# Kernel optimization log

Hardware: AMD Instinct MI355X
Metric: run time of the kernel (lower is better)

## Reference

```python
import jax, jax.numpy as jnp
import numpy as np


def setup_inputs() -> dict:
    key = jax.random.key(0)
    k1, k2, k3 = jax.random.split(key, 3)
    B, H, I, O, Dp1 = 4, 2048, 1024, 1024, 4  # degree=3 -> degree+1=4
    x = jax.random.normal(k1, (B, H, I, Dp1), dtype=jnp.float32)
    weight = 0.1 * jax.random.normal(k2, (O, Dp1), dtype=jnp.float32)
    weighted_sum = 0.1 * jax.random.normal(k3, (O, I), dtype=jnp.float32)
    return {"x": x, "weight": weight, "weighted_sum": weighted_sum}


def reference(x, weight, weighted_sum):
    # Original: weights[o,i,d] = weighted_sum[o,i] * weight[o,d];
    #           out[b,h,o] = sum_{i,d} x[b,h,i,d] * weights[o,i,d]
    # Fused 3-operand einsum avoids materializing the (O, I, D+1) intermediate.
    return jnp.einsum('bhid,oi,od->bho', x, weighted_sum, weight)
```

## Files before the change

### kernel.cpp

```cpp
#include <hip/hip_runtime.h>

typedef unsigned short u16;
typedef u16 u16x4 __attribute__((ext_vector_type(4)));
typedef float f32x4 __attribute__((ext_vector_type(4)));
typedef __bf16 bf16x8 __attribute__((ext_vector_type(8)));

#define M_DIM 8192
#define N_DIM 1024
#define K_DIM 4096

__device__ __forceinline__ u16 f2bf(float f) {
  unsigned u = __float_as_uint(f);
  u += 0x7FFFu + ((u >> 16) & 1u);
  return (u16)(u >> 16);
}

__global__ __launch_bounds__(256) void k_cvt(const float* __restrict__ x,
                                             u16* __restrict__ y) {
  long i = ((long)blockIdx.x * 256 + threadIdx.x) * 4;
  f32x4 a = *(const f32x4*)(x + i);
  u16x4 r;
  r[0] = f2bf(a[0]); r[1] = f2bf(a[1]); r[2] = f2bf(a[2]); r[3] = f2bf(a[3]);
  *(u16x4*)(y + i) = r;
}

__global__ __launch_bounds__(256) void k_w2(const float* __restrict__ w,
                                            const float* __restrict__ ws,
                                            u16* __restrict__ w2) {
  int idx = blockIdx.x * 256 + threadIdx.x;
  int o = idx >> 10;
  float s = ws[idx];
  f32x4 wv = *(const f32x4*)(w + o * 4);
  u16x4 r;
  r[0] = f2bf(s * wv[0]); r[1] = f2bf(s * wv[1]);
  r[2] = f2bf(s * wv[2]); r[3] = f2bf(s * wv[3]);
  *(u16x4*)(w2 + (size_t)idx * 4) = r;
}

typedef __attribute__((address_space(1))) const void gvoid_t;
typedef __attribute__((address_space(3))) void lvoid_t;
__device__ __forceinline__ void gll16(const void* g, void* l) {
  __builtin_amdgcn_global_load_lds((gvoid_t*)g, (lvoid_t*)l, 16, 0, 0);
}

__global__ __launch_bounds__(512) void k_gemm(const u16* __restrict__ A,
                                              const u16* __restrict__ Bt,
                                              float* __restrict__ C) {
  __shared__ u16 sA[128 * 64];
  __shared__ u16 sB[128 * 64];

  const int t    = threadIdx.x;
  const int lane = t & 63;
  const int wid  = t >> 6;
  const int m0   = blockIdx.y * 128;
  const int n0   = blockIdx.x * 128;

  const int s0 = t, s1 = t + 512;
  const int r0 = s0 >> 3, c0 = (s0 & 7) ^ (r0 & 7);
  const int r1 = s1 >> 3, c1 = (s1 & 7) ^ (r1 & 7);
  const u16* gA0 = A  + (size_t)(m0 + r0) * K_DIM + c0 * 8;
  const u16* gA1 = A  + (size_t)(m0 + r1) * K_DIM + c1 * 8;
  const u16* gB0 = Bt + (size_t)(n0 + r0) * K_DIM + c0 * 8;
  const u16* gB1 = Bt + (size_t)(n0 + r1) * K_DIM + c1 * 8;
  u16* lA0 = sA + s0 * 8;  u16* lA1 = sA + s1 * 8;
  u16* lB0 = sB + s0 * 8;  u16* lB1 = sB + s1 * 8;

  const int wm = (wid >> 1) * 32;
  const int wn = (wid & 1) * 64;
  const int fr = lane & 15;
  const int lc = lane >> 4;

  f32x4 acc[2][4];
#pragma unroll
  for (int i = 0; i < 2; i++)
#pragma unroll
    for (int j = 0; j < 4; j++) acc[i][j] = (f32x4){0.f, 0.f, 0.f, 0.f};

  for (int k0 = 0; k0 < K_DIM; k0 += 64) {
    gll16(gA0, lA0); gll16(gA1, lA1);
    gll16(gB0, lB0); gll16(gB1, lB1);
    gA0 += 64; gA1 += 64; gB0 += 64; gB1 += 64;
    __syncthreads();

#pragma unroll
    for (int ks = 0; ks < 2; ks++) {
      bf16x8 af[2], bf[4];
#pragma unroll
      for (int mi = 0; mi < 2; mi++) {
        int r  = wm + mi * 16 + fr;
        int pc = (ks * 4 + lc) ^ (r & 7);
        af[mi] = *(const bf16x8*)(sA + r * 64 + pc * 8);
      }
#pragma unroll
      for (int ni = 0; ni < 4; ni++) {
        int r  = wn + ni * 16 + fr;
        int pc = (ks * 4 + lc) ^ (r & 7);
        bf[ni] = *(const bf16x8*)(sB + r * 64 + pc * 8);
      }
#pragma unroll
      for (int mi = 0; mi < 2; mi++)
#pragma unroll
        for (int ni = 0; ni < 4; ni++)
          acc[mi][ni] = __builtin_amdgcn_mfma_f32_16x16x32_bf16(
              af[mi], bf[ni], acc[mi][ni], 0, 0, 0);
    }
    __syncthreads();
  }

  const int cr = (lane >> 4) * 4;
  const int cc = lane & 15;
#pragma unroll
  for (int mi = 0; mi < 2; mi++)
#pragma unroll
    for (int ni = 0; ni < 4; ni++) {
      float* cp = C + (size_t)(m0 + wm + mi * 16 + cr) * N_DIM +
                  (n0 + wn + ni * 16 + cc);
#pragma unroll
      for (int r = 0; r < 4; r++) cp[(size_t)r * N_DIM] = acc[mi][ni][r];
    }
}

extern "C" void kernel_launch(void* const* d_in, const int* in_sizes, int n_in,
                              void* d_out, int out_size, void* d_ws, size_t ws_size,
                              hipStream_t stream) {
  const float* x  = (const float*)d_in[0];
  const float* w  = (const float*)d_in[1];
  const float* ws = (const float*)d_in[2];
  float* out = (float*)d_out;

  u16* xbf = (u16*)d_ws;
  u16* w2  = xbf + (size_t)M_DIM * K_DIM;

  k_cvt<<<32768, 256, 0, stream>>>(x, xbf);
  k_w2<<<4096, 256, 0, stream>>>(w, ws, w2);

  dim3 grid(N_DIM / 128, M_DIM / 128);
  k_gemm<<<grid, 512, 0, stream>>>(xbf, w2, out);
}
```

Baseline: 279.5 us.

## Split K across wave pairs in GEMM with LDS reduction of partial sums

The GEMM block now gives each wave a 64x64 output tile instead of 32x64, with the two halves of each 64-wide K slice handled by separate wave groups. The partial accumulators are then summed through shared memory before the store. This halves the LDS fragment loads per MFMA and raises register-level reuse. In exchange it adds a reduction step, more accumulator registers, a larger shared buffer (64KB) and a launch-bounds occupancy hint.

After: 279.8 us. About the same (+0.1%).

```diff
diff --git a/kernel.cpp b/kernel.cpp
--- a/kernel.cpp
+++ b/kernel.cpp
@@ -43,11 +43,12 @@
   __builtin_amdgcn_global_load_lds((gvoid_t*)g, (lvoid_t*)l, 16, 0, 0);
 }
 
-__global__ __launch_bounds__(512) void k_gemm(const u16* __restrict__ A,
-                                              const u16* __restrict__ Bt,
-                                              float* __restrict__ C) {
-  __shared__ u16 sA[128 * 64];
-  __shared__ u16 sB[128 * 64];
+__global__ __launch_bounds__(512, 4) void k_gemm(const u16* __restrict__ A,
+                                                 const u16* __restrict__ Bt,
+                                                 float* __restrict__ C) {
+  __shared__ u16 smem[32768];
+  u16* sA = smem;
+  u16* sB = smem + 8192;
 
   const int t    = threadIdx.x;
   const int lane = t & 63;
@@ -65,14 +66,15 @@
   u16* lA0 = sA + s0 * 8;  u16* lA1 = sA + s1 * 8;
   u16* lB0 = sB + s0 * 8;  u16* lB1 = sB + s1 * 8;
 
-  const int wm = (wid >> 1) * 32;
-  const int wn = (wid & 1) * 64;
+  const int kh = wid >> 2;
+  const int wm = (wid & 1) * 64;
+  const int wn = ((wid >> 1) & 1) * 64;
   const int fr = lane & 15;
   const int lc = lane >> 4;
 
-  f32x4 acc[2][4];
+  f32x4 acc[4][4];
 #pragma unroll
-  for (int i = 0; i < 2; i++)
+  for (int i = 0; i < 4; i++)
 #pragma unroll
     for (int j = 0; j < 4; j++) acc[i][j] = (f32x4){0.f, 0.f, 0.f, 0.f};
 
@@ -82,42 +84,58 @@
     gA0 += 64; gA1 += 64; gB0 += 64; gB1 += 64;
     __syncthreads();
 
+    bf16x8 af[4], bf[4];
 #pragma unroll
-    for (int ks = 0; ks < 2; ks++) {
-      bf16x8 af[2], bf[4];
+    for (int mi = 0; mi < 4; mi++) {
+      int r  = wm + mi * 16 + fr;
+      int pc = (kh * 4 + lc) ^ (r & 7);
+      af[mi] = *(const bf16x8*)(sA + r * 64 + pc * 8);
+    }
 #pragma unroll
-      for (int mi = 0; mi < 2; mi++) {
-        int r  = wm + mi * 16 + fr;
-        int pc = (ks * 4 + lc) ^ (r & 7);
-        af[mi] = *(const bf16x8*)(sA + r * 64 + pc * 8);
-      }
+    for (int ni = 0; ni < 4; ni++) {
+      int r  = wn + ni * 16 + fr;
+      int pc = (kh * 4 + lc) ^ (r & 7);
+      bf[ni] = *(const bf16x8*)(sB + r * 64 + pc * 8);
+    }
 #pragma unroll
-      for (int ni = 0; ni < 4; ni++) {
-        int r  = wn + ni * 16 + fr;
-        int pc = (ks * 4 + lc) ^ (r & 7);
-        bf[ni] = *(const bf16x8*)(sB + r * 64 + pc * 8);
-      }
+    for (int mi = 0; mi < 4; mi++)
 #pragma unroll
-      for (int mi = 0; mi < 2; mi++)
-#pragma unroll
-        for (int ni = 0; ni < 4; ni++)
-          acc[mi][ni] = __builtin_amdgcn_mfma_f32_16x16x32_bf16(
-              af[mi], bf[ni], acc[mi][ni], 0, 0, 0);
-    }
+      for (int ni = 0; ni < 4; ni++)
+        acc[mi][ni] = __builtin_amdgcn_mfma_f32_16x16x32_bf16(
+            af[mi], bf[ni], acc[mi][ni], 0, 0, 0);
     __syncthreads();
   }
 
-  const int cr = (lane >> 4) * 4;
-  const int cc = lane & 15;
+  float* red = (float*)smem;
+  if (wid >= 4) {
+    float* dst = red + (wid - 4) * 4096 + lane * 4;
 #pragma unroll
-  for (int mi = 0; mi < 2; mi++)
+    for (int mi = 0; mi < 4; mi++)
 #pragma unroll
-    for (int ni = 0; ni < 4; ni++) {
-      float* cp = C + (size_t)(m0 + wm + mi * 16 + cr) * N_DIM +
-                  (n0 + wn + ni * 16 + cc);
+      for (int ni = 0; ni < 4; ni++)
+        *(f32x4*)(dst + (mi * 4 + ni) * 256) = acc[mi][ni];
+  }
+  __syncthreads();
+  if (wid < 4) {
+    float* src = red + wid * 4096 + lane * 4;
 #pragma unroll
-      for (int r = 0; r < 4; r++) cp[(size_t)r * N_DIM] = acc[mi][ni][r];
-    }
+    for (int mi = 0; mi < 4; mi++)
+#pragma unroll
+      for (int ni = 0; ni < 4; ni++)
+        acc[mi][ni] += *(const f32x4*)(src + (mi * 4 + ni) * 256);
+
+    const int cr = (lane >> 4) * 4;
+    const int cc = lane & 15;
+#pragma unroll
+    for (int mi = 0; mi < 4; mi++)
+#pragma unroll
+      for (int ni = 0; ni < 4; ni++) {
+        float* cp = C + (size_t)(m0 + wm + mi * 16 + cr) * N_DIM +
+                    (n0 + wn + ni * 16 + cc);
+#pragma unroll
+        for (int r = 0; r < 4; r++) cp[(size_t)r * N_DIM] = acc[mi][ni][r];
+      }
+  }
 }
 
 extern "C" void kernel_launch(void* const* d_in, const int* in_sizes, int n_in,
```
